# Kernel optimization log

Measured on AMD Instinct MI355X. Metric: run time of the kernel, lower is better.

Reference implementation:

```python
import jax, jax.numpy as jnp
import numpy as np
from jax.ops import segment_sum

N = 20000; IN = 256; HID = 256; Z = 64; DEC_H = 64; E = 120000; NEG = 5
BETA = 1.0; LN_EPS = 1e-5; TAU_MIN = 1e-4


def setup_inputs() -> dict:
    rng = np.random.default_rng(0)
    a = rng.integers(0, N, E)
    b = (a + 1 + rng.integers(0, N - 1, E)) % N  # guarantees a != b
    lo, hi = np.minimum(a, b), np.maximum(a, b)
    pos_edge = jnp.asarray(np.stack([lo, hi]), dtype=jnp.int32)          # [2,E], i<j single copy
    edge_index = jnp.asarray(np.stack([np.concatenate([lo, hi]),
                                       np.concatenate([hi, lo])]), dtype=jnp.int32)  # [2,2E] undirected
    neg_edge = jnp.asarray(rng.integers(0, N, (2, NEG * E)), dtype=jnp.int32)
    ks = jax.random.split(jax.random.key(0), 12)
    p = lambda i, shape, s=0.02: (jax.random.normal(ks[i], shape, jnp.float32) * s)
    return dict(
        x=p(0, (N, IN), 1.0), eps=p(1, (N, Z), 1.0),
        edge_index=edge_index, pos_edge=pos_edge, neg_edge=neg_edge,
        W1=p(2, (IN, HID)), b1=jnp.zeros((HID,), jnp.float32),
        g1=jnp.ones((HID,), jnp.float32), bt1=jnp.zeros((HID,), jnp.float32),
        Wmu=p(3, (HID, Z)), bmu=jnp.zeros((Z,), jnp.float32),
        Wlv=p(4, (HID, Z)), blv=jnp.zeros((Z,), jnp.float32),
        Wd1=p(5, (Z, Z)), bd1=jnp.zeros((Z,), jnp.float32),
        Wd2=p(6, (Z, Z)), bd2=jnp.zeros((Z,), jnp.float32),
        Wa=p(7, (4 * Z, DEC_H)), ba=jnp.zeros((DEC_H,), jnp.float32),
        Wb=p(8, (DEC_H, 1)), bb=jnp.zeros((1,), jnp.float32),
        tau=jnp.array(1.0, jnp.float32))


def _gcn_plain(h, src, dst, W, b):
    # GCNConv(add_self_loops=False, normalize=False): unnormalized scatter-add
    m = h @ W                                   # [N,F]
    return segment_sum(m[src], dst, num_segments=N) + b


def _gcn_norm(h, src, dst, W, b):
    # GCNConv defaults: self loops + symmetric normalization
    loops = jnp.arange(N, dtype=src.dtype)
    s = jnp.concatenate([src, loops]); d = jnp.concatenate([dst, loops])
    deg = segment_sum(jnp.ones_like(d, jnp.float32), d, num_segments=N)  # in-degree incl self
    dis = jax.lax.rsqrt(jnp.maximum(deg, 1.0))
    norm = dis[s] * dis[d]                      # [Emsg+N]
    m = h @ W
    return segment_sum(m[s] * norm[:, None], d, num_segments=N) + b


def _layernorm(h, g, bt):
    mu = jnp.mean(h, axis=-1, keepdims=True)
    var = jnp.mean((h - mu) ** 2, axis=-1, keepdims=True)
    return (h - mu) * jax.lax.rsqrt(var + LN_EPS) * g + bt


def _forward(x, eps, edge_index, pos_edge, neg_edge, W1, b1, g1, bt1, Wmu, bmu,
             Wlv, blv, Wd1, bd1, Wd2, bd2, Wa, ba, Wb, bb, tau):
    src, dst = edge_index[0], edge_index[1]
    # Encoder (dropout inactive: eval-mode reference)
    h1 = jax.nn.relu(_layernorm(_gcn_plain(x, src, dst, W1, b1), g1, bt1))
    mu = _gcn_plain(h1, src, dst, Wmu, bmu)
    logvar = _gcn_plain(h1, src, dst, Wlv, blv)
    z = mu + eps * jnp.exp(0.5 * logvar)
    # EdgeDecoder: 2 normalized GCN passes over positive (i<j) edges only
    ps, pd = pos_edge[0], pos_edge[1]
    h = jax.nn.relu(_gcn_norm(z, ps, pd, Wd1, bd1))
    h = jax.nn.relu(_gcn_norm(h, ps, pd, Wd2, bd2))
    # edge gather -> concat features -> MLP
    eu = jnp.concatenate([pos_edge[0], neg_edge[0]])
    ev = jnp.concatenate([pos_edge[1], neg_edge[1]])
    hu, hv = h[eu], h[ev]                        # [Ep+En, Z]
    phi = jnp.concatenate([hu, hv, jnp.abs(hu - hv), hu * hv], axis=-1)  # [Ep+En, 4Z]
    logits = (jax.nn.relu(phi @ Wa + ba) @ Wb + bb)[:, 0]
    logits = logits / jnp.clip(tau, TAU_MIN)
    # weighted BCE-with-logits; pos_weight = #neg/#pos = NEG
    n_pos = pos_edge.shape[1]; n_neg = neg_edge.shape[1]
    labels = jnp.concatenate([jnp.ones((n_pos,), jnp.float32), jnp.zeros((n_neg,), jnp.float32)])
    pw = jnp.float32(n_neg) / jnp.float32(n_pos)
    recon = -jnp.mean(pw * labels * jax.nn.log_sigmoid(logits)
                      + (1.0 - labels) * jax.nn.log_sigmoid(-logits))
    kl = -0.5 * jnp.mean(1.0 + logvar - mu ** 2 - jnp.exp(logvar))
    loss = recon + BETA * kl
    return loss, recon, kl


def reference(x, eps, edge_index, pos_edge, neg_edge, W1, b1, g1, bt1, Wmu, bmu,
              Wlv, blv, Wd1, bd1, Wd2, bd2, Wa, ba, Wb, bb, tau):
    return _forward(x, eps, edge_index, pos_edge, neg_edge, W1, b1, g1, bt1, Wmu,
                    bmu, Wlv, blv, Wd1, bd1, Wd2, bd2, Wa, ba, Wb, bb, tau)
```

## Files before the change

kernel.cpp:

```cpp
#include <hip/hip_runtime.h>
#include <hip/hip_bf16.h>
#include <hip/hip_fp16.h>
#include <math.h>

#define N_NODES 20000
#define E2      240000
#define EP      120000
#define ENEG    600000
#define ETOT    720000
#define NTILE   11250
#define POSTILE 1875
#define EMLP_BLOCKS 512
#define DEC_BLOCKS 1280
#define NCHUNK  20

#define WA_B  64
#define W1T_B 256
#define WML_B 128
#define UV_B  2813
#define HA_B  938
#define HP_B  469
#define FA_B  938
#define FP_B  469
#define FMM_SCATTER (FA_B + FP_B)
#define FMM_MM 2500

typedef __attribute__((ext_vector_type(8))) short bf16x8;
typedef __attribute__((ext_vector_type(8))) _Float16 f16x8;
typedef __attribute__((ext_vector_type(4))) float f32x4;

__device__ __forceinline__ float logsigf(float x) {
    return fminf(x, 0.0f) - log1pf(expf(-fabsf(x)));
}

__device__ __forceinline__ unsigned short f2bf(float f) {
    unsigned u = __float_as_uint(f);
    u += 0x7FFF + ((u >> 16) & 1);
    return (unsigned short)(u >> 16);
}

__device__ __forceinline__ unsigned short f2h(float f) {
    return __half_as_ushort(__float2half(f));
}

__device__ __forceinline__ float bflo(unsigned u) { return __uint_as_float(u << 16); }
__device__ __forceinline__ float bfhi(unsigned u) { return __uint_as_float(u & 0xFFFF0000u); }

__device__ __forceinline__ void store_out(float v, float* p) { *p = v; }
__device__ __forceinline__ void store_out(float v, unsigned short* p) { *p = f2bf(v); }
__device__ __forceinline__ void store_out(float v, __half* p) { *p = __float2half(v); }
__device__ __forceinline__ float load_in(const float* p) { return *p; }
__device__ __forceinline__ float load_in(const unsigned short* p) {
    return __uint_as_float(((unsigned)*p) << 16);
}
__device__ __forceinline__ float load_in(const __half* p) { return __half2float(*p); }

__device__ __forceinline__ int2 ldnt_int2(const int2* p) {
    const long long raw = __builtin_nontemporal_load((const long long*)p);
    int2 r; r.x = (int)(unsigned)(raw & 0xFFFFFFFFll); r.y = (int)(raw >> 32);
    return r;
}
__device__ __forceinline__ void stnt_int2(int2* p, int2 v) {
    const long long raw = ((long long)(unsigned)v.y << 32) | (unsigned)v.x;
    __builtin_nontemporal_store(raw, (long long*)p);
}

union I4H { int4 i; __half2 h[4]; f16x8 f; };

__device__ __forceinline__ f16x8 make_ad16(int4 a, int4 b) {
    I4H ua, ub, r;
    ua.i = a; ub.i = b;
#pragma unroll
    for (int k = 0; k < 4; ++k) r.h[k] = __habs2(__hsub2(ua.h[k], ub.h[k]));
    return r.f;
}

__device__ __forceinline__ f16x8 make_pr16(int4 a, int4 b) {
    I4H ua, ub, r;
    ua.i = a; ub.i = b;
#pragma unroll
    for (int k = 0; k < 4; ++k) r.h[k] = __hmul2(ua.h[k], ub.h[k]);
    return r.f;
}

__global__ void k_prep_csr(const float* __restrict__ Wa, unsigned short* __restrict__ WaT,
                           const float* __restrict__ W1, unsigned short* __restrict__ W1T,
                           const float* __restrict__ Wmu, const float* __restrict__ Wlv,
                           unsigned short* __restrict__ WmlT,
                           const int* __restrict__ pos, const int* __restrict__ neg,
                           int2* __restrict__ uv,
                           const int* __restrict__ e_dst, int* __restrict__ cntA,
                           const int* __restrict__ pd, int* __restrict__ cntP) {
    const int b = blockIdx.x, tid = threadIdx.x;
    if (b < WA_B) {
        const int idx = b * 256 + tid;
        const int j    = idx & 7;
        const int lane = (idx >> 3) & 63;
        const int fi   = idx >> 9;
        const int ks = fi & 7, nt = fi >> 3;
        const int quad = lane >> 4, l15 = lane & 15;
        const int n  = nt * 16 + l15;
        const int kp = ks * 32 + quad * 8 + j;
        const int part = kp >> 6;
        const int d = ((kp >> 3) & 3) * 16 + ((kp >> 5) & 1) * 8 + (kp & 7);
        WaT[idx] = f2h(Wa[(part * 64 + d) * 64 + n]);
    } else if (b < WA_B + W1T_B) {
        const int idx = (b - WA_B) * 256 + tid;
        const int n = idx >> 8, k = idx & 255;
        W1T[idx] = f2bf(W1[k * 256 + n]);
    } else if (b < WA_B + W1T_B + WML_B) {
        const int idx = (b - WA_B - W1T_B) * 256 + tid;
        const int n = idx >> 8, k = idx & 255;
        const float* W = (n & 1) ? Wlv : Wmu;
        WmlT[idx] = f2bf(W[k * 64 + (n >> 1)]);
    } else if (b < WA_B + W1T_B + WML_B + UV_B) {
        const int j = (b - WA_B - W1T_B - WML_B) * 256 + tid;
        if (j < ETOT) {
            int u, v;
            if (j < EP) { u = pos[j]; v = pos[EP + j]; }
            else        { u = neg[j - EP]; v = neg[ENEG + (j - EP)]; }
            stnt_int2(&uv[j], make_int2(u, v));
        }
    } else if (b < WA_B + W1T_B + WML_B + UV_B + HA_B) {
        const int e = (b - WA_B - W1T_B - WML_B - UV_B) * 256 + tid;
        if (e < E2) atomicAdd(&cntA[e_dst[e]], 1);
    } else {
        const int e = (b - WA_B - W1T_B - WML_B - UV_B - HA_B) * 256 + tid;
        if (e < EP) atomicAdd(&cntP[pd[e]], 1);
    }
}

__global__ __launch_bounds__(1024) void k_scan_par(const int* __restrict__ cntA,
                                                   int* __restrict__ rsA,
                                                   int* __restrict__ curA,
                                                   const int* __restrict__ cntP,
                                                   int* __restrict__ rsP,
                                                   int* __restrict__ curP,
                                                   float* __restrict__ dis) {
    const int arr = blockIdx.x / NCHUNK;
    const int c   = blockIdx.x % NCHUNK;
    const int* cnt = arr ? cntP : cntA;
    int* rs  = arr ? rsP  : rsA;
    int* cur = arr ? curP : curA;
    const int tid = threadIdx.x, lane = tid & 63, wid = tid >> 6;
    __shared__ int wred[16];

    int p = 0;
    for (int i = tid; i < c * 1024; i += 1024) p += cnt[i];
    for (int o = 32; o > 0; o >>= 1) p += __shfl_xor(p, o, 64);
    if (lane == 0) wred[wid] = p;
    __syncthreads();
    int prefix = 0;
#pragma unroll
    for (int k = 0; k < 16; ++k) prefix += wred[k];
    __syncthreads();

    const int i = c * 1024 + tid;
    const int v = (i < N_NODES) ? cnt[i] : 0;
    int x = v;
#pragma unroll
    for (int d = 1; d < 64; d <<= 1) {
        const int t = __shfl_up(x, d, 64);
        if (lane >= d) x += t;
    }
    if (lane == 63) wred[wid] = x;
    __syncthreads();
    int wexc = 0, tot = 0;
#pragma unroll
    for (int k = 0; k < 16; ++k) { if (k < wid) wexc += wred[k]; tot += wred[k]; }
    const int excl = prefix + wexc + x - v;
    if (i < N_NODES) {
        rs[i] = excl; cur[i] = excl;
        if (arr) dis[i] = rsqrtf((float)v + 1.0f);
    }
    if (c == NCHUNK - 1 && tid == 0) rs[N_NODES] = prefix + tot;
}

__global__ __launch_bounds__(256) void k_finish_mm(
        const int* __restrict__ e_src, const int* __restrict__ e_dst,
        int* __restrict__ curA, int* __restrict__ adjA,
        const int* __restrict__ ps, const int* __restrict__ pd,
        int* __restrict__ curP, int* __restrict__ adjP,
        const float* __restrict__ x, const unsigned short* __restrict__ W1T,
        unsigned short* __restrict__ m1) {
    __shared__ unsigned short sA[32 * 264];
    const int b = blockIdx.x, tid = threadIdx.x;
    if (b < FA_B) {
        const int e = b * 256 + tid;
        if (e < E2) {
            const int p = atomicAdd(&curA[e_dst[e]], 1);
            adjA[p] = e_src[e];
        }
        return;
    }
    if (b < FMM_SCATTER) {
        const int e = (b - FA_B) * 256 + tid;
        if (e < EP) {
            const int p = atomicAdd(&curP[pd[e]], 1);
            adjP[p] = ps[e];
        }
        return;
    }
    const int mb = (b - FMM_SCATTER) >> 2, nb = (b - FMM_SCATTER) & 3;
    const int w = tid >> 6, lane = tid & 63;
    const int l15 = lane & 15, quad = lane >> 4;

    for (int i = tid; i < 2048; i += 256) {
        const int row = i >> 6, kc = (i & 63) << 2;
        const float4 xv = *(const float4*)&x[((long)mb * 32 + row) * 256 + kc];
        union { unsigned short s[4]; unsigned long long ll; } pk;
        pk.s[0] = f2bf(xv.x); pk.s[1] = f2bf(xv.y);
        pk.s[2] = f2bf(xv.z); pk.s[3] = f2bf(xv.w);
        *(unsigned long long*)&sA[row * 264 + kc] = pk.ll;
    }

    bf16x8 breg[8];
#pragma unroll
    for (int ks = 0; ks < 8; ++ks)
        breg[ks] = *(const bf16x8*)&W1T[((nb * 64 + w * 16 + l15) << 8) + ks * 32 + quad * 8];
    __syncthreads();

    f32x4 acc[2];
    acc[0] = (f32x4){0.f,0.f,0.f,0.f};
    acc[1] = (f32x4){0.f,0.f,0.f,0.f};
#pragma unroll
    for (int ks = 0; ks < 8; ++ks) {
#pragma unroll
        for (int st = 0; st < 2; ++st) {
            const bf16x8 af = *(const bf16x8*)&sA[(st * 16 + l15) * 264 + ks * 32 + quad * 8];
            acc[st] = __builtin_amdgcn_mfma_f32_16x16x32_bf16(af, breg[ks], acc[st], 0, 0, 0);
        }
    }
#pragma unroll
    for (int st = 0; st < 2; ++st)
#pragma unroll
        for (int r = 0; r < 4; ++r)
            m1[((long)mb * 32 + st * 16 + quad * 4 + r) * 256 + nb * 64 + w * 16 + l15] =
                f2bf(acc[st][r]);
}

__global__ __launch_bounds__(256) void k_gather_ln(const unsigned short* __restrict__ m1,
                                                   const int* __restrict__ rs,
                                                   const int* __restrict__ adj,
                                                   const float* __restrict__ b1,
                                                   const float* __restrict__ g1,
                                                   const float* __restrict__ bt1,
                                                   unsigned short* __restrict__ h1) {
    const int wid = threadIdx.x >> 6, lane = threadIdx.x & 63;
    const int n = blockIdx.x * 4 + wid;
    const int beg = rs[n], end = rs[n + 1];
    float4 a0 = {0.f,0.f,0.f,0.f}, a1 = {0.f,0.f,0.f,0.f};
    float4 a2 = {0.f,0.f,0.f,0.f}, a3 = {0.f,0.f,0.f,0.f};
    int j = beg;
    for (; j + 7 < end; j += 8) {
        const int s0 = adj[j],     s1 = adj[j + 1], s2 = adj[j + 2], s3 = adj[j + 3];
        const int s4 = adj[j + 4], s5 = adj[j + 5], s6 = adj[j + 6], s7 = adj[j + 7];
        const uint2 u0 = *(const uint2*)(m1 + (long)s0 * 256 + lane * 4);
        const uint2 u1 = *(const uint2*)(m1 + (long)s1 * 256 + lane * 4);
        const uint2 u2 = *(const uint2*)(m1 + (long)s2 * 256 + lane * 4);
        const uint2 u3 = *(const uint2*)(m1 + (long)s3 * 256 + lane * 4);
        const uint2 u4 = *(const uint2*)(m1 + (long)s4 * 256 + lane * 4);
        const uint2 u5 = *(const uint2*)(m1 + (long)s5 * 256 + lane * 4);
        const uint2 u6 = *(const uint2*)(m1 + (long)s6 * 256 + lane * 4);
        const uint2 u7 = *(const uint2*)(m1 + (long)s7 * 256 + lane * 4);
        a0.x += bflo(u0.x); a0.y += bfhi(u0.x); a0.z += bflo(u0.y); a0.w += bfhi(u0.y);
        a1.x += bflo(u1.x); a1.y += bfhi(u1.x); a1.z += bflo(u1.y); a1.w += bfhi(u1.y);
        a2.x += bflo(u2.x); a2.y += bfhi(u2.x); a2.z += bflo(u2.y); a2.w += bfhi(u2.y);
        a3.x += bflo(u3.x); a3.y += bfhi(u3.x); a3.z += bflo(u3.y); a3.w += bfhi(u3.y);
        a0.x += bflo(u4.x); a0.y += bfhi(u4.x); a0.z += bflo(u4.y); a0.w += bfhi(u4.y);
        a1.x += bflo(u5.x); a1.y += bfhi(u5.x); a1.z += bflo(u5.y); a1.w += bfhi(u5.y);
        a2.x += bflo(u6.x); a2.y += bfhi(u6.x); a2.z += bflo(u6.y); a2.w += bfhi(u6.y);
        a3.x += bflo(u7.x); a3.y += bfhi(u7.x); a3.z += bflo(u7.y); a3.w += bfhi(u7.y);
    }
    for (; j + 3 < end; j += 4) {
        const int s0 = adj[j], s1 = adj[j + 1], s2 = adj[j + 2], s3 = adj[j + 3];
        const uint2 u0 = *(const uint2*)(m1 + (long)s0 * 256 + lane * 4);
        const uint2 u1 = *(const uint2*)(m1 + (long)s1 * 256 + lane * 4);
        const uint2 u2 = *(const uint2*)(m1 + (long)s2 * 256 + lane * 4);
        const uint2 u3 = *(const uint2*)(m1 + (long)s3 * 256 + lane * 4);
        a0.x += bflo(u0.x); a0.y += bfhi(u0.x); a0.z += bflo(u0.y); a0.w += bfhi(u0.y);
        a1.x += bflo(u1.x); a1.y += bfhi(u1.x); a1.z += bflo(u1.y); a1.w += bfhi(u1.y);
        a2.x += bflo(u2.x); a2.y += bfhi(u2.x); a2.z += bflo(u2.y); a2.w += bfhi(u2.y);
        a3.x += bflo(u3.x); a3.y += bfhi(u3.x); a3.z += bflo(u3.y); a3.w += bfhi(u3.y);
    }
    for (; j < end; ++j) {
        const int s0 = adj[j];
        const uint2 u = *(const uint2*)(m1 + (long)s0 * 256 + lane * 4);
        a0.x += bflo(u.x); a0.y += bfhi(u.x); a0.z += bflo(u.y); a0.w += bfhi(u.y);
    }
    float4 v;
    const float4 b = *(const float4*)(b1 + lane * 4);
    v.x = (a0.x + a1.x) + (a2.x + a3.x) + b.x;
    v.y = (a0.y + a1.y) + (a2.y + a3.y) + b.y;
    v.z = (a0.z + a1.z) + (a2.z + a3.z) + b.z;
    v.w = (a0.w + a1.w) + (a2.w + a3.w) + b.w;
    float s  = v.x + v.y + v.z + v.w;
    float sq = v.x * v.x + v.y * v.y + v.z * v.z + v.w * v.w;
    for (int o = 32; o > 0; o >>= 1) {
        s  += __shfl_xor(s, o, 64);
        sq += __shfl_xor(sq, o, 64);
    }
    const float mean = s * (1.0f / 256.0f);
    const float var  = sq * (1.0f / 256.0f) - mean * mean;
    const float rsv = rsqrtf(var + 1e-5f);
    const float4 g  = *(const float4*)(g1 + lane * 4);
    const float4 bt = *(const float4*)(bt1 + lane * 4);
    union { unsigned short sh[4]; unsigned long long ll; } pk;
    pk.sh[0] = f2bf(fmaxf((v.x - mean) * rsv * g.x + bt.x, 0.f));
    pk.sh[1] = f2bf(fmaxf((v.y - mean) * rsv * g.y + bt.y, 0.f));
    pk.sh[2] = f2bf(fmaxf((v.z - mean) * rsv * g.z + bt.z, 0.f));
    pk.sh[3] = f2bf(fmaxf((v.w - mean) * rsv * g.w + bt.w, 0.f));
    *(unsigned long long*)&h1[(long)n * 256 + lane * 4] = pk.ll;
}

__global__ __launch_bounds__(256) void k_mm_hml_mfma(const unsigned short* __restrict__ h1,
                                                     const unsigned short* __restrict__ WmlT,
                                                     unsigned short* __restrict__ hml) {
    __shared__ unsigned short sA[32 * 264];
    const int tid = threadIdx.x;
    const int w = tid >> 6, lane = tid & 63;
    const int l15 = lane & 15, quad = lane >> 4;
    const int mb = blockIdx.x >> 1, nb = blockIdx.x & 1;

    for (int i = tid; i < 1024; i += 256) {
        const int row = i >> 5, kc = (i & 31) << 3;
        *(int4*)&sA[row * 264 + kc] = *(const int4*)&h1[((long)mb * 32 + row) * 256 + kc];
    }

    bf16x8 breg[8];
#pragma unroll
    for (int ks = 0; ks < 8; ++ks)
        breg[ks] = *(const bf16x8*)&WmlT[((nb * 64 + w * 16 + l15) << 8) + ks * 32 + quad * 8];
    __syncthreads();

    f32x4 acc[2];
    acc[0] = (f32x4){0.f,0.f,0.f,0.f};
    acc[1] = (f32x4){0.f,0.f,0.f,0.f};
#pragma unroll
    for (int ks = 0; ks < 8; ++ks) {
#pragma unroll
        for (int st = 0; st < 2; ++st) {
            const bf16x8 af = *(const bf16x8*)&sA[(st * 16 + l15) * 264 + ks * 32 + quad * 8];
            acc[st] = __builtin_amdgcn_mfma_f32_16x16x32_bf16(af, breg[ks], acc[st], 0, 0, 0);
        }
    }
#pragma unroll
    for (int st = 0; st < 2; ++st)
#pragma unroll
        for (int r = 0; r < 4; ++r)
            hml[((long)mb * 32 + st * 16 + quad * 4 + r) * 128 + nb * 64 + w * 16 + l15] =
                f2bf(acc[st][r]);
}

__global__ __launch_bounds__(256) void k_gather_mulv(const unsigned short* __restrict__ hml,
                                                     const int* __restrict__ rs,
                                                     const int* __restrict__ adj,
                                                     const float* __restrict__ bmu,
                                                     const float* __restrict__ blv,
                                                     const float* __restrict__ eps,
                                                     unsigned short* __restrict__ z,
                                                     double* __restrict__ kl_part) {
    __shared__ double sKL[4];
    const int wid = threadIdx.x >> 6, lane = threadIdx.x & 63;
    const int n = blockIdx.x * 4 + wid;
    const int beg = rs[n], end = rs[n + 1];
    float m0 = 0.f, m1_ = 0.f, m2 = 0.f, m3 = 0.f;
    float l0 = 0.f, l1 = 0.f, l2 = 0.f, l3 = 0.f;
    int j = beg;
    for (; j + 7 < end; j += 8) {
        const int s0 = adj[j],     s1 = adj[j + 1], s2 = adj[j + 2], s3 = adj[j + 3];
        const int s4 = adj[j + 4], s5 = adj[j + 5], s6 = adj[j + 6], s7 = adj[j + 7];
        const unsigned u0 = *(const unsigned*)(hml + (long)s0 * 128 + lane * 2);
        const unsigned u1 = *(const unsigned*)(hml + (long)s1 * 128 + lane * 2);
        const unsigned u2 = *(const unsigned*)(hml + (long)s2 * 128 + lane * 2);
        const unsigned u3 = *(const unsigned*)(hml + (long)s3 * 128 + lane * 2);
        const unsigned u4 = *(const unsigned*)(hml + (long)s4 * 128 + lane * 2);
        const unsigned u5 = *(const unsigned*)(hml + (long)s5 * 128 + lane * 2);
        const unsigned u6 = *(const unsigned*)(hml + (long)s6 * 128 + lane * 2);
        const unsigned u7 = *(const unsigned*)(hml + (long)s7 * 128 + lane * 2);
        m0 += bflo(u0); l0 += bfhi(u0);
        m1_ += bflo(u1); l1 += bfhi(u1);
        m2 += bflo(u2); l2 += bfhi(u2);
        m3 += bflo(u3); l3 += bfhi(u3);
        m0 += bflo(u4); l0 += bfhi(u4);
        m1_ += bflo(u5); l1 += bfhi(u5);
        m2 += bflo(u6); l2 += bfhi(u6);
        m3 += bflo(u7); l3 += bfhi(u7);
    }
    for (; j + 3 < end; j += 4) {
        const int s0 = adj[j], s1 = adj[j + 1], s2 = adj[j + 2], s3 = adj[j + 3];
        const unsigned u0 = *(const unsigned*)(hml + (long)s0 * 128 + lane * 2);
        const unsigned u1 = *(const unsigned*)(hml + (long)s1 * 128 + lane * 2);
        const unsigned u2 = *(const unsigned*)(hml + (long)s2 * 128 + lane * 2);
        const unsigned u3 = *(const unsigned*)(hml + (long)s3 * 128 + lane * 2);
        m0 += bflo(u0); l0 += bfhi(u0);
        m1_ += bflo(u1); l1 += bfhi(u1);
        m2 += bflo(u2); l2 += bfhi(u2);
        m3 += bflo(u3); l3 += bfhi(u3);
    }
    for (; j < end; ++j) {
        const int s0 = adj[j];
        const unsigned u0 = *(const unsigned*)(hml + (long)s0 * 128 + lane * 2);
        m0 += bflo(u0); l0 += bfhi(u0);
    }
    const float mu = (m0 + m1_) + (m2 + m3) + bmu[lane];
    const float lv = (l0 + l1) + (l2 + l3) + blv[lane];
    z[(long)n * 64 + lane] = f2bf(mu + eps[(long)n * 64 + lane] * expf(0.5f * lv));
    float term = 1.0f + lv - mu * mu - expf(lv);
    for (int o = 32; o > 0; o >>= 1) term += __shfl_xor(term, o, 64);
    if (lane == 0) sKL[wid] = (double)term;
    __syncthreads();
    if (threadIdx.x == 0)
        kl_part[blockIdx.x] = sKL[0] + sKL[1] + sKL[2] + sKL[3];
}

template <typename IN, typename OUT>
__global__ __launch_bounds__(256) void k_dec_fused(const IN* __restrict__ feat,
                                                   const int* __restrict__ rs,
                                                   const int* __restrict__ adj,
                                                   const float* __restrict__ dis,
                                                   const float* __restrict__ Wd,
                                                   const float* __restrict__ bd,
                                                   OUT* __restrict__ out) {
    __shared__ float sW[64 * 64];
    __shared__ float rows[4][64];
    const int tid = threadIdx.x;
    {
        const float4* w4 = (const float4*)Wd;
        float4* sw4 = (float4*)sW;
        for (int i = tid; i < 1024; i += 256) sw4[i] = w4[i];
    }
    const int wid = tid >> 6, lane = tid & 63;
    const float bdl = bd[lane];
    __syncthreads();

    for (int g = blockIdx.x; g < (N_NODES + 3) / 4; g += DEC_BLOCKS) {
        const int n = g * 4 + wid;
        const int beg = rs[n], end = rs[n + 1];
        float a0 = 0.f, a1 = 0.f, a2 = 0.f, a3 = 0.f;
        int j = beg;
        for (; j + 3 < end; j += 4) {
            const int s0 = adj[j], s1 = adj[j + 1], s2 = adj[j + 2], s3 = adj[j + 3];
            a0 += load_in(&feat[(long)s0 * 64 + lane]) * dis[s0];
            a1 += load_in(&feat[(long)s1 * 64 + lane]) * dis[s1];
            a2 += load_in(&feat[(long)s2 * 64 + lane]) * dis[s2];
            a3 += load_in(&feat[(long)s3 * 64 + lane]) * dis[s3];
        }
        for (; j < end; ++j) {
            const int s0 = adj[j];
            a0 += load_in(&feat[(long)s0 * 64 + lane]) * dis[s0];
        }
        const float dn = dis[n];
        rows[wid][lane] = ((a0 + a1) + (a2 + a3)) * dn
                        + load_in(&feat[(long)n * 64 + lane]) * dn * dn;
        float acc = 0.f;
        for (int k = 0; k < 64; k += 4) {
            const float4 a = *(const float4*)&rows[wid][k];
            acc += a.x * sW[(k+0)*64+lane] + a.y * sW[(k+1)*64+lane]
                 + a.z * sW[(k+2)*64+lane] + a.w * sW[(k+3)*64+lane];
        }
        store_out(fmaxf(acc + bdl, 0.f), &out[(long)n * 64 + lane]);
    }
}

__global__ __launch_bounds__(256, 2) void k_edge_mlp_mfma(
        const __half* __restrict__ h2,
        const int2* __restrict__ uv,
        const unsigned short* __restrict__ WaT,
        const float* __restrict__ ba,
        const float* __restrict__ Wb,
        const float* __restrict__ bb,
        const float* __restrict__ tau,
        double* __restrict__ recon_part) {
    __shared__ float sBa[64], sWb[64];
    __shared__ double sRed[4];
    const int tid = threadIdx.x;
    const int w = tid >> 6, lane = tid & 63;
    const int l15 = lane & 15, quad = lane >> 4;

    if (tid < 64) { sBa[tid] = ba[tid]; sWb[tid] = Wb[tid]; }

    f16x8 areg[4][8];
#pragma unroll
    for (int nt = 0; nt < 4; ++nt)
#pragma unroll
        for (int ks = 0; ks < 8; ++ks)
            areg[nt][ks] = *(const f16x8*)&WaT[((((nt * 8 + ks) << 6) + lane) << 3)];

    const float bb0 = bb[0];
    const float itau = 1.0f / fmaxf(tau[0], 1e-4f);
    __syncthreads();

    float lsum = 0.f;

    int t = blockIdx.x;
    const int slot = w * 16 + l15;
    int2 uvA = ldnt_int2(&uv[t * 64 + slot]);
    int4 hua = *(const int4*)(h2 + (long)uvA.x * 64 + quad * 16);
    int4 hub = *(const int4*)(h2 + (long)uvA.x * 64 + quad * 16 + 8);
    int4 hva = *(const int4*)(h2 + (long)uvA.y * 64 + quad * 16);
    int4 hvb = *(const int4*)(h2 + (long)uvA.y * 64 + quad * 16 + 8);
    int2 uvB = (t + EMLP_BLOCKS < NTILE) ? ldnt_int2(&uv[(t + EMLP_BLOCKS) * 64 + slot]) : uvA;

    for (; t < NTILE; t += EMLP_BLOCKS) {
        const int t2 = t + 2 * EMLP_BLOCKS;
        const int2 uvC = (t2 < NTILE) ? ldnt_int2(&uv[t2 * 64 + slot]) : uvB;

        int4 nhua = hua, nhub = hub, nhva = hva, nhvb = hvb;
        if (t + EMLP_BLOCKS < NTILE) {
            nhua = *(const int4*)(h2 + (long)uvB.x * 64 + quad * 16);
            nhub = *(const int4*)(h2 + (long)uvB.x * 64 + quad * 16 + 8);
            nhva = *(const int4*)(h2 + (long)uvB.y * 64 + quad * 16);
            nhvb = *(const int4*)(h2 + (long)uvB.y * 64 + quad * 16 + 8);
        }

        const f16x8 fad_a = make_ad16(hua, hva);
        const f16x8 fad_b = make_ad16(hub, hvb);
        const f16x8 fpr_a = make_pr16(hua, hva);
        const f16x8 fpr_b = make_pr16(hub, hvb);

        f32x4 acc[4];
#pragma unroll
        for (int nt = 0; nt < 4; ++nt) acc[nt] = (f32x4){0.f, 0.f, 0.f, 0.f};

        const f16x8 bhu_a = *(const f16x8*)&hua;
        const f16x8 bhu_b = *(const f16x8*)&hub;
        const f16x8 bhv_a = *(const f16x8*)&hva;
        const f16x8 bhv_b = *(const f16x8*)&hvb;

#pragma unroll
        for (int nt = 0; nt < 4; ++nt) {
            acc[nt] = __builtin_amdgcn_mfma_f32_16x16x32_f16(areg[nt][0], bhu_a, acc[nt], 0, 0, 0);
            acc[nt] = __builtin_amdgcn_mfma_f32_16x16x32_f16(areg[nt][1], bhu_b, acc[nt], 0, 0, 0);
            acc[nt] = __builtin_amdgcn_mfma_f32_16x16x32_f16(areg[nt][2], bhv_a, acc[nt], 0, 0, 0);
            acc[nt] = __builtin_amdgcn_mfma_f32_16x16x32_f16(areg[nt][3], bhv_b, acc[nt], 0, 0, 0);
            acc[nt] = __builtin_amdgcn_mfma_f32_16x16x32_f16(areg[nt][4], fad_a, acc[nt], 0, 0, 0);
            acc[nt] = __builtin_amdgcn_mfma_f32_16x16x32_f16(areg[nt][5], fad_b, acc[nt], 0, 0, 0);
            acc[nt] = __builtin_amdgcn_mfma_f32_16x16x32_f16(areg[nt][6], fpr_a, acc[nt], 0, 0, 0);
            acc[nt] = __builtin_amdgcn_mfma_f32_16x16x32_f16(areg[nt][7], fpr_b, acc[nt], 0, 0, 0);
        }

        float s = 0.f;
#pragma unroll
        for (int nt = 0; nt < 4; ++nt) {
            const float4 b4 = *(const float4*)&sBa[nt * 16 + quad * 4];
            const float4 w4 = *(const float4*)&sWb[nt * 16 + quad * 4];
            s += fmaxf(acc[nt][0] + b4.x, 0.f) * w4.x
               + fmaxf(acc[nt][1] + b4.y, 0.f) * w4.y
               + fmaxf(acc[nt][2] + b4.z, 0.f) * w4.z
               + fmaxf(acc[nt][3] + b4.w, 0.f) * w4.w;
        }
        s += __shfl_xor(s, 16, 64);
        s += __shfl_xor(s, 32, 64);
        if (lane < 16) {
            const float logit = (s + bb0) * itau;
            lsum += (t < POSTILE) ? 5.0f * logsigf(logit) : logsigf(-logit);
        }

        hua = nhua; hub = nhub; hva = nhva; hvb = nhvb;
        uvB = uvC;
    }

    for (int o = 32; o > 0; o >>= 1) lsum += __shfl_xor(lsum, o, 64);
    if (lane == 0) sRed[w] = (double)lsum;
    __syncthreads();
    if (tid == 0)
        recon_part[blockIdx.x] = sRed[0] + sRed[1] + sRed[2] + sRed[3];
}

__global__ __launch_bounds__(1024) void k_final(const double* __restrict__ kl_part,
                                                const double* __restrict__ recon_part,
                                                float* __restrict__ out) {
    __shared__ double sK[16], sR[16];
    const int tid = threadIdx.x, lane = tid & 63, wid = tid >> 6;
    double kl = 0.0, rc = 0.0;
    for (int i = tid; i < 5000; i += 1024) kl += kl_part[i];
    for (int i = tid; i < EMLP_BLOCKS; i += 1024) rc += recon_part[i];
    for (int o = 32; o > 0; o >>= 1) {
        kl += __shfl_xor(kl, o, 64);
        rc += __shfl_xor(rc, o, 64);
    }
    if (lane == 0) { sK[wid] = kl; sR[wid] = rc; }
    __syncthreads();
    if (tid == 0) {
        double K = 0.0, R = 0.0;
        for (int i = 0; i < 16; ++i) { K += sK[i]; R += sR[i]; }
        const double recon = -R / (double)ETOT;
        const double klv = -0.5 * K / ((double)N_NODES * 64.0);
        out[0] = (float)(recon + klv);
        out[1] = (float)recon;
        out[2] = (float)klv;
    }
}

extern "C" void kernel_launch(void* const* d_in, const int* in_sizes, int n_in,
                              void* d_out, int out_size, void* d_ws, size_t ws_size,
                              hipStream_t stream) {
    const float* x   = (const float*)d_in[0];
    const float* eps = (const float*)d_in[1];
    const int* EI    = (const int*)d_in[2];
    const int* pos   = (const int*)d_in[3];
    const int* neg   = (const int*)d_in[4];
    const float* W1  = (const float*)d_in[5];
    const float* b1  = (const float*)d_in[6];
    const float* g1  = (const float*)d_in[7];
    const float* bt1 = (const float*)d_in[8];
    const float* Wmu = (const float*)d_in[9];
    const float* bmu = (const float*)d_in[10];
    const float* Wlv = (const float*)d_in[11];
    const float* blv = (const float*)d_in[12];
    const float* Wd1 = (const float*)d_in[13];
    const float* bd1 = (const float*)d_in[14];
    const float* Wd2 = (const float*)d_in[15];
    const float* bd2 = (const float*)d_in[16];
    const float* Wa  = (const float*)d_in[17];
    const float* ba  = (const float*)d_in[18];
    const float* Wb  = (const float*)d_in[19];
    const float* bb  = (const float*)d_in[20];
    const float* tau = (const float*)d_in[21];

    const int* e_src = EI;
    const int* e_dst = EI + E2;
    const int* ps = pos;
    const int* pd = pos + EP;

    float* ws = (float*)d_ws;
    unsigned short* m1bf  = (unsigned short*)ws;
    unsigned short* hmlbf = (unsigned short*)ws;
    __half* hdec = (__half*)(ws + 2560000);
    __half* h2   = (__half*)(ws + 3840000);
    unsigned short* h1bf = (unsigned short*)(ws + 5120000);
    unsigned short* z    = (unsigned short*)(ws + 10240000);
    float* dis   = ws + 11520000;
    unsigned short* WaT = (unsigned short*)(ws + 11540004);
    int* cntA = (int*)(ws + 11548200);
    int* cntP = (int*)(ws + 11568200);
    int* rsA  = (int*)(ws + 11588200);
    int* adjA = (int*)(ws + 11608204);
    int* rsP  = (int*)(ws + 11848204);
    int* adjP = (int*)(ws + 11868208);
    int2* uv  = (int2*)(ws + 11988208);
    double* kl_part    = (double*)(ws + 13428208);
    double* recon_part = (double*)(ws + 13438208);
    unsigned short* W1T  = (unsigned short*)(ws + 13440256);
    unsigned short* WmlT = (unsigned short*)(ws + 13473024);
    int* curA = (int*)(ws + 13489408);
    int* curP = (int*)(ws + 13509408);

    hipMemsetAsync(cntA, 0, 2 * N_NODES * 4, stream);

    k_prep_csr<<<WA_B + W1T_B + WML_B + UV_B + HA_B + HP_B, 256, 0, stream>>>(
        Wa, WaT, W1, W1T, Wmu, Wlv, WmlT, pos, neg, uv, e_dst, cntA, pd, cntP);
    k_scan_par<<<2 * NCHUNK, 1024, 0, stream>>>(cntA, rsA, curA, cntP, rsP, curP, dis);
    k_finish_mm<<<FMM_SCATTER + FMM_MM, 256, 0, stream>>>(
        e_src, e_dst, curA, adjA, ps, pd, curP, adjP, x, W1T, m1bf);

    k_gather_ln<<<5000, 256, 0, stream>>>(m1bf, rsA, adjA, b1, g1, bt1, h1bf);
    k_mm_hml_mfma<<<1250, 256, 0, stream>>>(h1bf, WmlT, hmlbf);
    k_gather_mulv<<<5000, 256, 0, stream>>>(hmlbf, rsA, adjA, bmu, blv, eps, z, kl_part);

    k_dec_fused<unsigned short, __half><<<DEC_BLOCKS, 256, 0, stream>>>(
        z, rsP, adjP, dis, Wd1, bd1, hdec);
    k_dec_fused<__half, __half><<<DEC_BLOCKS, 256, 0, stream>>>(
        hdec, rsP, adjP, dis, Wd2, bd2, h2);

    k_edge_mlp_mfma<<<EMLP_BLOCKS, 256, 0, stream>>>(h2, uv, WaT, ba, Wb, bb, tau, recon_part);
    k_final<<<1, 1024, 0, stream>>>(kl_part, recon_part, (float*)d_out);
}
```

Baseline: 298.8 us.

## Fuse gather-layernorm with mu/logvar projection MFMA into one kernel

Merges the neighbor-gather + LayerNorm kernel with the following h1·[Wmu|Wlv] MFMA GEMM. Each block keeps its 4 normalized rows in shared memory, zero-pads the tile to 16 rows, and runs the 16x16x32 MFMA directly, writing only the 128-wide hml output. This removes the h1 round trip through global memory and one launch. In exchange, three quarters of every MFMA tile is padding, each block reloads the weight fragments from global or cache, and a __syncthreads is added after the gather.

```diff
diff --git a/kernel.cpp b/kernel.cpp
--- a/kernel.cpp
+++ b/kernel.cpp
@@ -239,14 +239,23 @@
                 f2bf(acc[st][r]);
 }
 
-__global__ __launch_bounds__(256) void k_gather_ln(const unsigned short* __restrict__ m1,
-                                                   const int* __restrict__ rs,
-                                                   const int* __restrict__ adj,
-                                                   const float* __restrict__ b1,
-                                                   const float* __restrict__ g1,
-                                                   const float* __restrict__ bt1,
-                                                   unsigned short* __restrict__ h1) {
-    const int wid = threadIdx.x >> 6, lane = threadIdx.x & 63;
+__global__ __launch_bounds__(256) void k_gather_ln_ml(const unsigned short* __restrict__ m1,
+                                                      const int* __restrict__ rs,
+                                                      const int* __restrict__ adj,
+                                                      const float* __restrict__ b1,
+                                                      const float* __restrict__ g1,
+                                                      const float* __restrict__ bt1,
+                                                      const unsigned short* __restrict__ WmlT,
+                                                      unsigned short* __restrict__ hml) {
+    __shared__ unsigned short sA[16 * 264];
+    const int tid = threadIdx.x;
+    const int wid = tid >> 6, lane = tid & 63;
+
+    {
+        unsigned long long* z0 = (unsigned long long*)&sA[4 * 264];
+        for (int i = tid; i < 792; i += 256) z0[i] = 0ULL;
+    }
+
     const int n = blockIdx.x * 4 + wid;
     const int beg = rs[n], end = rs[n + 1];
     float4 a0 = {0.f,0.f,0.f,0.f}, a1 = {0.f,0.f,0.f,0.f};
@@ -310,46 +319,30 @@
     pk.sh[1] = f2bf(fmaxf((v.y - mean) * rsv * g.y + bt.y, 0.f));
     pk.sh[2] = f2bf(fmaxf((v.z - mean) * rsv * g.z + bt.z, 0.f));
     pk.sh[3] = f2bf(fmaxf((v.w - mean) * rsv * g.w + bt.w, 0.f));
-    *(unsigned long long*)&h1[(long)n * 256 + lane * 4] = pk.ll;
-}
-
-__global__ __launch_bounds__(256) void k_mm_hml_mfma(const unsigned short* __restrict__ h1,
-                                                     const unsigned short* __restrict__ WmlT,
-                                                     unsigned short* __restrict__ hml) {
-    __shared__ unsigned short sA[32 * 264];
-    const int tid = threadIdx.x;
-    const int w = tid >> 6, lane = tid & 63;
+    *(unsigned long long*)&sA[wid * 264 + lane * 4] = pk.ll;
+    __syncthreads();
+
     const int l15 = lane & 15, quad = lane >> 4;
-    const int mb = blockIdx.x >> 1, nb = blockIdx.x & 1;
-
-    for (int i = tid; i < 1024; i += 256) {
-        const int row = i >> 5, kc = (i & 31) << 3;
-        *(int4*)&sA[row * 264 + kc] = *(const int4*)&h1[((long)mb * 32 + row) * 256 + kc];
-    }
-
-    bf16x8 breg[8];
-#pragma unroll
-    for (int ks = 0; ks < 8; ++ks)
-        breg[ks] = *(const bf16x8*)&WmlT[((nb * 64 + w * 16 + l15) << 8) + ks * 32 + quad * 8];
-    __syncthreads();
-
-    f32x4 acc[2];
-    acc[0] = (f32x4){0.f,0.f,0.f,0.f};
-    acc[1] = (f32x4){0.f,0.f,0.f,0.f};
+    f32x4 acc0 = (f32x4){0.f,0.f,0.f,0.f};
+    f32x4 acc1 = (f32x4){0.f,0.f,0.f,0.f};
+    const int c0 = (wid * 2 + 0) * 16 + l15;
+    const int c1 = (wid * 2 + 1) * 16 + l15;
 #pragma unroll
     for (int ks = 0; ks < 8; ++ks) {
-#pragma unroll
-        for (int st = 0; st < 2; ++st) {
-            const bf16x8 af = *(const bf16x8*)&sA[(st * 16 + l15) * 264 + ks * 32 + quad * 8];
-            acc[st] = __builtin_amdgcn_mfma_f32_16x16x32_bf16(af, breg[ks], acc[st], 0, 0, 0);
-        }
-    }
-#pragma unroll
-    for (int st = 0; st < 2; ++st)
-#pragma unroll
-        for (int r = 0; r < 4; ++r)
-            hml[((long)mb * 32 + st * 16 + quad * 4 + r) * 128 + nb * 64 + w * 16 + l15] =
-                f2bf(acc[st][r]);
+        const bf16x8 af = *(const bf16x8*)&sA[l15 * 264 + ks * 32 + quad * 8];
+        const bf16x8 b0 = *(const bf16x8*)&WmlT[(c0 << 8) + ks * 32 + quad * 8];
+        const bf16x8 b1f = *(const bf16x8*)&WmlT[(c1 << 8) + ks * 32 + quad * 8];
+        acc0 = __builtin_amdgcn_mfma_f32_16x16x32_bf16(af, b0, acc0, 0, 0, 0);
+        acc1 = __builtin_amdgcn_mfma_f32_16x16x32_bf16(af, b1f, acc1, 0, 0, 0);
+    }
+    if (quad == 0) {
+        const long nb4 = (long)blockIdx.x * 4;
+#pragma unroll
+        for (int r = 0; r < 4; ++r) {
+            hml[(nb4 + r) * 128 + c0] = f2bf(acc0[r]);
+            hml[(nb4 + r) * 128 + c1] = f2bf(acc1[r]);
+        }
+    }
 }
 
 __global__ __launch_bounds__(256) void k_gather_mulv(const unsigned short* __restrict__ hml,
@@ -626,10 +619,9 @@
 
     float* ws = (float*)d_ws;
     unsigned short* m1bf  = (unsigned short*)ws;
-    unsigned short* hmlbf = (unsigned short*)ws;
     __half* hdec = (__half*)(ws + 2560000);
     __half* h2   = (__half*)(ws + 3840000);
-    unsigned short* h1bf = (unsigned short*)(ws + 5120000);
+    unsigned short* hmlbf = (unsigned short*)(ws + 5120000);
     unsigned short* z    = (unsigned short*)(ws + 10240000);
     float* dis   = ws + 11520000;
     unsigned short* WaT = (unsigned short*)(ws + 11540004);
@@ -655,8 +647,7 @@
     k_finish_mm<<<FMM_SCATTER + FMM_MM, 256, 0, stream>>>(
         e_src, e_dst, curA, adjA, ps, pd, curP, adjP, x, W1T, m1bf);
 
-    k_gather_ln<<<5000, 256, 0, stream>>>(m1bf, rsA, adjA, b1, g1, bt1, h1bf);
-    k_mm_hml_mfma<<<1250, 256, 0, stream>>>(h1bf, WmlT, hmlbf);
+    k_gather_ln_ml<<<5000, 256, 0, stream>>>(m1bf, rsA, adjA, b1, g1, bt1, WmlT, hmlbf);
     k_gather_mulv<<<5000, 256, 0, stream>>>(hmlbf, rsA, adjA, bmu, blv, eps, z, kl_part);
 
     k_dec_fused<unsigned short, __half><<<DEC_BLOCKS, 256, 0, stream>>>(
```

Result: slower. 323.1 us (+8.1%).
